# Optimization experiments

Hardware: AMD Instinct MI355X
Metric: run time of the kernel (lower is better)

Reference implementation:

```python
import jax, jax.numpy as jnp
import numpy as np

NUM_QUERIES = 10000
NUM_CLASSES = 2048
IOU_THRESH = 0.5


def setup_inputs() -> dict:
    key = jax.random.key(0)
    k1, k2, k3, k4 = jax.random.split(key, 4)
    return {
        "pred_logits": jax.random.normal(k1, (1, NUM_QUERIES, NUM_CLASSES), dtype=jnp.float32),
        "pred_boxes": jax.random.uniform(k2, (1, NUM_QUERIES, 4), dtype=jnp.float32),
        "cls_logits": jax.random.normal(k3, (1, NUM_CLASSES), dtype=jnp.float32),
        "target_sizes": jax.random.randint(k4, (1, 2), 480, 1333, dtype=jnp.int64),
    }


def box_cxcywh_to_xyxy(b):
    cx, cy, w, h = b[..., 0], b[..., 1], b[..., 2], b[..., 3]
    return jnp.stack([cx - 0.5 * w, cy - 0.5 * h, cx + 0.5 * w, cy + 0.5 * h], axis=-1)


def nms_keep(boxes, scores, iou_thresh):
    """Greedy NMS; returns a boolean keep mask over the N boxes (xyxy)."""
    n = boxes.shape[0]
    order = jnp.argsort(-scores)
    bs = boxes[order]  # [N,4] sorted by score desc
    areas = jnp.clip(bs[:, 2] - bs[:, 0], 0.0) * jnp.clip(bs[:, 3] - bs[:, 1], 0.0)
    idx = jnp.arange(n)

    def body(i, state):
        keep_s, active = state
        alive = active[i]
        keep_s = keep_s.at[i].set(alive)
        # IoU of box i against all boxes
        lt = jnp.maximum(bs[i, :2], bs[:, :2])
        rb = jnp.minimum(bs[i, 2:], bs[:, 2:])
        wh = jnp.clip(rb - lt, 0.0)
        inter = wh[:, 0] * wh[:, 1]
        iou = inter / (areas[i] + areas - inter)
        suppress = (iou > iou_thresh) & (idx > i) & alive
        return keep_s, active & (~suppress)

    keep_s, _ = jax.lax.fori_loop(
        0, n, body, (jnp.zeros(n, dtype=bool), jnp.ones(n, dtype=bool))
    )
    # map back from sorted order to original order
    return jnp.zeros(n, dtype=bool).at[order].set(keep_s)


def reference(pred_logits, pred_boxes, cls_logits, target_sizes):
    # class scores / labels
    prob = jax.nn.softmax(pred_logits, axis=-1)          # [B,Q,C]
    scores = prob.max(axis=-1)                           # [B,Q]
    labels = prob.argmax(axis=-1)                        # [B,Q]
    cls_preds = jnp.argmax(cls_logits, axis=1)           # [B]

    # boxes: cxcywh -> xyxy, clamp to [0,1], scale to image size
    boxes = jnp.clip(box_cxcywh_to_xyxy(pred_boxes), 0.0, 1.0)  # [B,Q,4]
    ts = target_sizes.astype(jnp.float32)
    img_h, img_w = ts[:, 0], ts[:, 1]
    scale_fct = jnp.stack([img_w, img_h, img_w, img_h], axis=1)  # [B,4]
    boxes = boxes * scale_fct[:, None, :]

    # greedy NMS on batch 0 (module only supports this path for B=1)
    keep = nms_keep(boxes[0], scores.reshape(-1), IOU_THRESH)    # [Q] bool

    return scores[0], labels[0], boxes[0], keep, cls_preds
```

## Files before the change

### kernel.cpp

```cpp
#include <hip/hip_runtime.h>
#include <stdint.h>

#define NQ 10000
#define NC 2048
#define NW 157
#define IOU_TH 0.5f


__global__ __launch_bounds__(256) void k_scores(const float* __restrict__ logits,
        float* __restrict__ out_scores, float* __restrict__ out_labels,
        float* __restrict__ ws_scores) {
    int wave = threadIdx.x >> 6;
    int lane = threadIdx.x & 63;
    int q = blockIdx.x * 4 + wave;
    if (q >= NQ) return;
    const float* row = logits + (size_t)q * NC;
    float4 v[8];
    float m = -3.4e38f;
    int am = 0;
    #pragma unroll
    for (int k = 0; k < 8; k++) {
        int idx = k * 256 + lane * 4;
        v[k] = *(const float4*)(row + idx);
        if (v[k].x > m) { m = v[k].x; am = idx; }
        if (v[k].y > m) { m = v[k].y; am = idx + 1; }
        if (v[k].z > m) { m = v[k].z; am = idx + 2; }
        if (v[k].w > m) { m = v[k].w; am = idx + 3; }
    }
    #pragma unroll
    for (int off = 32; off >= 1; off >>= 1) {
        float om = __shfl_xor(m, off);
        int   oa = __shfl_xor(am, off);
        if (om > m || (om == m && oa < am)) { m = om; am = oa; }
    }
    float s = 0.f;
    #pragma unroll
    for (int k = 0; k < 8; k++) {
        s += expf(v[k].x - m);
        s += expf(v[k].y - m);
        s += expf(v[k].z - m);
        s += expf(v[k].w - m);
    }
    #pragma unroll
    for (int off = 32; off >= 1; off >>= 1) s += __shfl_xor(s, off);
    if (lane == 0) {
        float sc = 1.0f / s;
        out_scores[q] = sc;
        out_labels[q] = (float)am;
        ws_scores[q]  = sc;
    }
}

__global__ __launch_bounds__(256) void k_cls(const float* __restrict__ cls,
                                             float* __restrict__ out) {
    float m = -3.4e38f; int am = 0x7fffffff;
    for (int idx = threadIdx.x; idx < NC; idx += 256) {
        float x = cls[idx];
        if (x > m) { m = x; am = idx; }
    }
    int lane = threadIdx.x & 63, wave = threadIdx.x >> 6;
    #pragma unroll
    for (int off = 32; off >= 1; off >>= 1) {
        float om = __shfl_xor(m, off); int oa = __shfl_xor(am, off);
        if (om > m || (om == m && oa < am)) { m = om; am = oa; }
    }
    __shared__ float sm[4]; __shared__ int sa[4];
    if (lane == 0) { sm[wave] = m; sa[wave] = am; }
    __syncthreads();
    if (threadIdx.x == 0) {
        for (int w = 1; w < 4; w++)
            if (sm[w] > m || (sm[w] == m && sa[w] < am)) { m = sm[w]; am = sa[w]; }
        out[0] = (float)am;
    }
}

__global__ __launch_bounds__(256) void k_boxes(const float* __restrict__ pb,
        const int* __restrict__ ts, float* __restrict__ out_boxes,
        float* __restrict__ boxes4, int* __restrict__ rank) {
    #pragma clang fp contract(off)
    int i = blockIdx.x * 256 + threadIdx.x;
    if (i >= NQ) return;
    rank[i] = 0;
    int a0 = ts[0], a1 = ts[1];
    int ih, iw;
    if (a1 == 0) { ih = a0; iw = ts[2]; } else { ih = a0; iw = a1; }
    float sh = (float)ih, sw = (float)iw;
    float4 b = *(const float4*)(pb + i * 4);
    float x1 = b.x - 0.5f * b.z;
    float y1 = b.y - 0.5f * b.w;
    float x2 = b.x + 0.5f * b.z;
    float y2 = b.y + 0.5f * b.w;
    x1 = fminf(fmaxf(x1, 0.f), 1.f) * sw;
    y1 = fminf(fmaxf(y1, 0.f), 1.f) * sh;
    x2 = fminf(fmaxf(x2, 0.f), 1.f) * sw;
    y2 = fminf(fmaxf(y2, 0.f), 1.f) * sh;
    float4 o = make_float4(x1, y1, x2, y2);
    *(float4*)(out_boxes + i * 4) = o;
    *(float4*)(boxes4 + i * 4) = o;
}

__global__ __launch_bounds__(256) void k_count(const float* __restrict__ scores,
                                               int* __restrict__ rank) {
    __shared__ float sc[2000];
    int jbase = blockIdx.y * 2000;
    int jn = min(2000, NQ - jbase);
    for (int t = threadIdx.x; t < jn; t += 256) sc[t] = scores[jbase + t];
    __syncthreads();
    int i = blockIdx.x * 256 + threadIdx.x;
    if (i >= NQ) return;
    float si = scores[i];
    int cnt = 0;
    for (int jj = 0; jj < jn; jj++) {
        float sj = sc[jj];
        int j = jbase + jj;
        cnt += (sj > si) || (sj == si && j < i);
    }
    if (cnt) atomicAdd(&rank[i], cnt);
}

__global__ __launch_bounds__(256) void k_scatter(const float* __restrict__ boxes4,
        const int* __restrict__ rank, int* __restrict__ order,
        float* __restrict__ sx1, float* __restrict__ sy1,
        float* __restrict__ sx2, float* __restrict__ sy2,
        float* __restrict__ sarea) {
    #pragma clang fp contract(off)
    int i = blockIdx.x * 256 + threadIdx.x;
    if (i >= NQ) return;
    int r = rank[i];
    order[r] = i;
    float4 b = *(const float4*)(boxes4 + i * 4);
    sx1[r] = b.x; sy1[r] = b.y; sx2[r] = b.z; sy2[r] = b.w;
    sarea[r] = fmaxf(b.z - b.x, 0.f) * fmaxf(b.w - b.y, 0.f);
}

__global__ __launch_bounds__(64) void k_mask(const float* __restrict__ sx1,
        const float* __restrict__ sy1, const float* __restrict__ sx2,
        const float* __restrict__ sy2, const float* __restrict__ sarea,
        unsigned long long* __restrict__ mask) {
    #pragma clang fp contract(off)
    int rb = blockIdx.x, cb = blockIdx.y;
    if (cb < rb) return;
    int t = threadIdx.x;
    __shared__ float cx1[64], cy1[64], cx2[64], cy2[64], ca[64];
    int j0 = cb * 64 + t;
    if (j0 < NQ) { cx1[t]=sx1[j0]; cy1[t]=sy1[j0]; cx2[t]=sx2[j0]; cy2[t]=sy2[j0]; ca[t]=sarea[j0]; }
    __syncthreads();
    int i = rb * 64 + t;
    if (i >= NQ) return;
    float xi1 = sx1[i], yi1 = sy1[i], xi2 = sx2[i], yi2 = sy2[i], ai = sarea[i];
    int ncol = min(64, NQ - cb * 64);
    unsigned long long word = 0;
    for (int jj = 0; jj < ncol; jj++) {
        int j = cb * 64 + jj;
        float lx = fmaxf(xi1, cx1[jj]);
        float ly = fmaxf(yi1, cy1[jj]);
        float rx = fminf(xi2, cx2[jj]);
        float ry = fminf(yi2, cy2[jj]);
        float w = fmaxf(rx - lx, 0.f);
        float h = fmaxf(ry - ly, 0.f);
        float inter = w * h;
        float denom = (ai + ca[jj]) - inter;
        float iou = inter / denom;
        bool sup = (iou > IOU_TH) && (j > i);
        word |= ((unsigned long long)(sup ? 1u : 0u)) << jj;
    }
    mask[(size_t)i * NW + cb] = word;
}

__global__ __launch_bounds__(256, 1) void k_scan(const unsigned long long* __restrict__ mask,
        const int* __restrict__ order, float* __restrict__ out_keep) {
    __shared__ unsigned long long rem[NW];
    __shared__ unsigned long long keepw[NW];
    __shared__ unsigned long long sh_kept;

    const int tid  = threadIdx.x;
    const int wave = tid >> 6;
    const int lane = tid & 63;

    for (int w = tid; w < NW; w += 256) rem[w] = 0;

    uint32_t dg_lo = 0, dg_hi = 0;
    if (wave == 0) {
        uint64_t dg = mask[(size_t)lane * NW + 0];
        dg_lo = (uint32_t)dg; dg_hi = (uint32_t)(dg >> 32);
    }
    __syncthreads();

    for (int c = 0; c < NW; c++) {
        if (wave == 0) {
            uint64_t t64 = rem[c];
            uint32_t clo = (uint32_t)__builtin_amdgcn_readfirstlane((int)(uint32_t)t64);
            uint32_t chi = (uint32_t)__builtin_amdgcn_readfirstlane((int)(uint32_t)(t64 >> 32));
            uint64_t cur = ((uint64_t)chi << 32) | clo;

            int nvalid = min(64, NQ - c * 64);
            if (nvalid < 64) cur |= (~0ull) << nvalid;

            uint64_t alive = ~cur;
            uint64_t kept  = 0;
            while (alive) {
                int b = (int)__builtin_ctzll(alive);
                uint32_t dlo = (uint32_t)__builtin_amdgcn_readlane((int)dg_lo, b);
                uint32_t dhi = (uint32_t)__builtin_amdgcn_readlane((int)dg_hi, b);
                uint64_t d = ((uint64_t)dhi << 32) | dlo;
                kept  |= 1ull << b;
                cur   |= d;
                alive &= ~(d | (1ull << b));
            }
            if (tid == 0) { sh_kept = kept; keepw[c] = cur; }
        }
        __syncthreads();

        uint64_t kt;
        {
            uint64_t t64 = sh_kept;
            uint32_t klo = (uint32_t)__builtin_amdgcn_readfirstlane((int)(uint32_t)t64);
            uint32_t khi = (uint32_t)__builtin_amdgcn_readfirstlane((int)(uint32_t)(t64 >> 32));
            kt = ((uint64_t)khi << 32) | klo;
        }

        uint64_t dg_n = 0;
        if (wave == 0 && c + 1 < NW) {
            int i2 = (c + 1) * 64 + lane;
            if (i2 < NQ) dg_n = mask[(size_t)i2 * NW + (c + 1)];
        }

        int w = c + 1 + tid;
        if (w < NW && kt) {
            const unsigned long long* base = mask + (size_t)c * 64 * NW + w;
            uint64_t acc = 0;
            uint64_t km = kt;
            while (km) {
                uint64_t a0 = 0, a1 = 0, a2 = 0, a3 = 0, a4 = 0, a5 = 0, a6 = 0, a7 = 0;
                if (km) { int r = (int)__builtin_ctzll(km); km &= km - 1; a0 = base[(size_t)r * NW]; }
                if (km) { int r = (int)__builtin_ctzll(km); km &= km - 1; a1 = base[(size_t)r * NW]; }
                if (km) { int r = (int)__builtin_ctzll(km); km &= km - 1; a2 = base[(size_t)r * NW]; }
                if (km) { int r = (int)__builtin_ctzll(km); km &= km - 1; a3 = base[(size_t)r * NW]; }
                if (km) { int r = (int)__builtin_ctzll(km); km &= km - 1; a4 = base[(size_t)r * NW]; }
                if (km) { int r = (int)__builtin_ctzll(km); km &= km - 1; a5 = base[(size_t)r * NW]; }
                if (km) { int r = (int)__builtin_ctzll(km); km &= km - 1; a6 = base[(size_t)r * NW]; }
                if (km) { int r = (int)__builtin_ctzll(km); km &= km - 1; a7 = base[(size_t)r * NW]; }
                acc |= (a0 | a1) | (a2 | a3) | ((a4 | a5) | (a6 | a7));
            }
            if (acc) rem[w] |= acc;
        }
        __syncthreads();

        if (wave == 0) { dg_lo = (uint32_t)dg_n; dg_hi = (uint32_t)(dg_n >> 32); }
    }

    for (int si = tid; si < NQ; si += 256) {
        unsigned long long kw = keepw[si >> 6];
        out_keep[order[si]] = ((kw >> (si & 63)) & 1ull) ? 0.f : 1.f;
    }
}

extern "C" void kernel_launch(void* const* d_in, const int* in_sizes, int n_in,
                              void* d_out, int out_size, void* d_ws, size_t ws_size,
                              hipStream_t stream) {
    const float* pred_logits = (const float*)d_in[0];
    const float* pred_boxes  = (const float*)d_in[1];
    const float* cls_logits  = (const float*)d_in[2];
    const int*   tsizes      = (const int*)d_in[3];

    float* out = (float*)d_out;
    float* out_scores = out;
    float* out_labels = out + 10000;
    float* out_boxes  = out + 20000;
    float* out_keep   = out + 60000;
    float* out_cls    = out + 70000;

    char* ws = (char*)d_ws;
    float* ws_scores = (float*)(ws + 0);
    int*   rank      = (int*)  (ws + 40000);
    float* boxes4    = (float*)(ws + 80000);
    float* sx1       = (float*)(ws + 240000);
    float* sy1       = (float*)(ws + 280000);
    float* sx2       = (float*)(ws + 320000);
    float* sy2       = (float*)(ws + 360000);
    float* sarea     = (float*)(ws + 400000);
    int*   order     = (int*)  (ws + 440000);
    unsigned long long* mask = (unsigned long long*)(ws + 480000);

    k_scores<<<2500, 256, 0, stream>>>(pred_logits, out_scores, out_labels, ws_scores);
    k_cls<<<1, 256, 0, stream>>>(cls_logits, out_cls);
    k_boxes<<<40, 256, 0, stream>>>(pred_boxes, tsizes, out_boxes, boxes4, rank);
    k_count<<<dim3(40, 5), 256, 0, stream>>>(ws_scores, rank);
    k_scatter<<<40, 256, 0, stream>>>(boxes4, rank, order, sx1, sy1, sx2, sy2, sarea);
    k_mask<<<dim3(157, 157), 64, 0, stream>>>(sx1, sy1, sx2, sy2, sarea, mask);
    k_scan<<<1, 256, 0, stream>>>(mask, order, out_keep);
}
```

Measured before the change: 497.3 us.

## Pipeline NMS scan by deferring far-column mask loads and prefetching next block

```diff
diff --git a/kernel.cpp b/kernel.cpp
--- a/kernel.cpp
+++ b/kernel.cpp
@@ -171,6 +171,8 @@
         const int* __restrict__ order, float* __restrict__ out_keep) {
     __shared__ unsigned long long rem[NW];
     __shared__ unsigned long long keepw[NW];
+    __shared__ unsigned long long dgbuf[2][64];
+    __shared__ unsigned long long ccbuf[2][64];
     __shared__ unsigned long long sh_kept;
 
     const int tid  = threadIdx.x;
@@ -179,74 +181,119 @@
 
     for (int w = tid; w < NW; w += 256) rem[w] = 0;
 
-    uint32_t dg_lo = 0, dg_hi = 0;
     if (wave == 0) {
-        uint64_t dg = mask[(size_t)lane * NW + 0];
-        dg_lo = (uint32_t)dg; dg_hi = (uint32_t)(dg >> 32);
+        const unsigned long long* rp = mask + (size_t)lane * NW;
+        dgbuf[0][lane] = rp[0];
+        ccbuf[0][lane] = rp[1];
     }
     __syncthreads();
 
+    uint64_t p0=0,p1=0,p2=0,p3=0,p4=0,p5=0,p6=0,p7=0;
+    uint64_t p8=0,p9=0,p10=0,p11=0,p12=0,p13=0,p14=0,p15=0;
+    uint64_t pextra = 0;
+    int pw = -1;
+
     for (int c = 0; c < NW; c++) {
+        uint64_t dn = 0, ccn = 0;
         if (wave == 0) {
+            if (c + 1 < NW) {
+                int i2 = (c + 1) * 64 + lane;
+                if (i2 < NQ) {
+                    const unsigned long long* rp = mask + (size_t)i2 * NW;
+                    dn = rp[c + 1];
+                    if (c + 2 < NW) ccn = rp[c + 2];
+                }
+            }
             uint64_t t64 = rem[c];
             uint32_t clo = (uint32_t)__builtin_amdgcn_readfirstlane((int)(uint32_t)t64);
             uint32_t chi = (uint32_t)__builtin_amdgcn_readfirstlane((int)(uint32_t)(t64 >> 32));
             uint64_t cur = ((uint64_t)chi << 32) | clo;
-
             int nvalid = min(64, NQ - c * 64);
             if (nvalid < 64) cur |= (~0ull) << nvalid;
+
+            uint64_t dgv = dgbuf[c & 1][lane];
+            uint32_t dvlo = (uint32_t)dgv, dvhi = (uint32_t)(dgv >> 32);
 
             uint64_t alive = ~cur;
             uint64_t kept  = 0;
             while (alive) {
                 int b = (int)__builtin_ctzll(alive);
-                uint32_t dlo = (uint32_t)__builtin_amdgcn_readlane((int)dg_lo, b);
-                uint32_t dhi = (uint32_t)__builtin_amdgcn_readlane((int)dg_hi, b);
+                uint32_t dlo = (uint32_t)__builtin_amdgcn_readlane((int)dvlo, b);
+                uint32_t dhi = (uint32_t)__builtin_amdgcn_readlane((int)dvhi, b);
                 uint64_t d = ((uint64_t)dhi << 32) | dlo;
                 kept  |= 1ull << b;
                 cur   |= d;
                 alive &= ~(d | (1ull << b));
             }
             if (tid == 0) { sh_kept = kept; keepw[c] = cur; }
+        } else {
+            if (pw >= 0) {
+                uint64_t pacc = ((p0|p1)|(p2|p3)) | ((p4|p5)|(p6|p7));
+                pacc |= ((p8|p9)|(p10|p11)) | ((p12|p13)|(p14|p15));
+                pacc |= pextra;
+                if (pacc) atomicOr(&rem[pw], (unsigned long long)pacc);
+            }
+            pw = -1;
         }
         __syncthreads();
 
-        uint64_t kt;
+        uint64_t kts;
         {
             uint64_t t64 = sh_kept;
             uint32_t klo = (uint32_t)__builtin_amdgcn_readfirstlane((int)(uint32_t)t64);
             uint32_t khi = (uint32_t)__builtin_amdgcn_readfirstlane((int)(uint32_t)(t64 >> 32));
-            kt = ((uint64_t)khi << 32) | klo;
+            kts = ((uint64_t)khi << 32) | klo;
         }
 
-        uint64_t dg_n = 0;
-        if (wave == 0 && c + 1 < NW) {
-            int i2 = (c + 1) * 64 + lane;
-            if (i2 < NQ) dg_n = mask[(size_t)i2 * NW + (c + 1)];
-        }
-
-        int w = c + 1 + tid;
-        if (w < NW && kt) {
-            const unsigned long long* base = mask + (size_t)c * 64 * NW + w;
-            uint64_t acc = 0;
-            uint64_t km = kt;
-            while (km) {
-                uint64_t a0 = 0, a1 = 0, a2 = 0, a3 = 0, a4 = 0, a5 = 0, a6 = 0, a7 = 0;
-                if (km) { int r = (int)__builtin_ctzll(km); km &= km - 1; a0 = base[(size_t)r * NW]; }
-                if (km) { int r = (int)__builtin_ctzll(km); km &= km - 1; a1 = base[(size_t)r * NW]; }
-                if (km) { int r = (int)__builtin_ctzll(km); km &= km - 1; a2 = base[(size_t)r * NW]; }
-                if (km) { int r = (int)__builtin_ctzll(km); km &= km - 1; a3 = base[(size_t)r * NW]; }
-                if (km) { int r = (int)__builtin_ctzll(km); km &= km - 1; a4 = base[(size_t)r * NW]; }
-                if (km) { int r = (int)__builtin_ctzll(km); km &= km - 1; a5 = base[(size_t)r * NW]; }
-                if (km) { int r = (int)__builtin_ctzll(km); km &= km - 1; a6 = base[(size_t)r * NW]; }
-                if (km) { int r = (int)__builtin_ctzll(km); km &= km - 1; a7 = base[(size_t)r * NW]; }
-                acc |= (a0 | a1) | (a2 | a3) | ((a4 | a5) | (a6 | a7));
-            }
-            if (acc) rem[w] |= acc;
+        if (wave == 0) {
+            if (c + 1 < NW) {
+                uint64_t ccv = ccbuf[c & 1][lane];
+                if ((kts >> lane) & 1ull) atomicOr(&rem[c + 1], (unsigned long long)ccv);
+                dgbuf[(c + 1) & 1][lane] = dn;
+                if (c + 2 < NW) ccbuf[(c + 1) & 1][lane] = ccn;
+            }
+        } else {
+            int w = c + 2 + (tid - 64);
+            if (kts && w < NW) {
+                const unsigned long long* base = mask + (size_t)(c * 64) * NW + w;
+                uint64_t km = kts;
+                int r_first = (int)__builtin_ctzll(km);
+                int r;
+                r = km ? (int)__builtin_ctzll(km) : r_first; if (km) km &= km - 1; p0  = base[(size_t)r * NW];
+                r = km ? (int)__builtin_ctzll(km) : r_first; if (km) km &= km - 1; p1  = base[(size_t)r * NW];
+                r = km ? (int)__builtin_ctzll(km) : r_first; if (km) km &= km - 1; p2  = base[(size_t)r * NW];
+                r = km ? (int)__builtin_ctzll(km) : r_first; if (km) km &= km - 1; p3  = base[(size_t)r * NW];
+                r = km ? (int)__builtin_ctzll(km) : r_first; if (km) km &= km - 1; p4  = base[(size_t)r * NW];
+                r = km ? (int)__builtin_ctzll(km) : r_first; if (km) km &= km - 1; p5  = base[(size_t)r * NW];
+                r = km ? (int)__builtin_ctzll(km) : r_first; if (km) km &= km - 1; p6  = base[(size_t)r * NW];
+                r = km ? (int)__builtin_ctzll(km) : r_first; if (km) km &= km - 1; p7  = base[(size_t)r * NW];
+                r = km ? (int)__builtin_ctzll(km) : r_first; if (km) km &= km - 1; p8  = base[(size_t)r * NW];
+                r = km ? (int)__builtin_ctzll(km) : r_first; if (km) km &= km - 1; p9  = base[(size_t)r * NW];
+                r = km ? (int)__builtin_ctzll(km) : r_first; if (km) km &= km - 1; p10 = base[(size_t)r * NW];
+                r = km ? (int)__builtin_ctzll(km) : r_first; if (km) km &= km - 1; p11 = base[(size_t)r * NW];
+                r = km ? (int)__builtin_ctzll(km) : r_first; if (km) km &= km - 1; p12 = base[(size_t)r * NW];
+                r = km ? (int)__builtin_ctzll(km) : r_first; if (km) km &= km - 1; p13 = base[(size_t)r * NW];
+                r = km ? (int)__builtin_ctzll(km) : r_first; if (km) km &= km - 1; p14 = base[(size_t)r * NW];
+                r = km ? (int)__builtin_ctzll(km) : r_first; if (km) km &= km - 1; p15 = base[(size_t)r * NW];
+                pextra = 0;
+                while (km) {
+                    uint64_t x0=0,x1=0,x2=0,x3=0,x4=0,x5=0,x6=0,x7=0;
+                    if (km) { r=(int)__builtin_ctzll(km); km&=km-1; x0=base[(size_t)r*NW]; }
+                    if (km) { r=(int)__builtin_ctzll(km); km&=km-1; x1=base[(size_t)r*NW]; }
+                    if (km) { r=(int)__builtin_ctzll(km); km&=km-1; x2=base[(size_t)r*NW]; }
+                    if (km) { r=(int)__builtin_ctzll(km); km&=km-1; x3=base[(size_t)r*NW]; }
+                    if (km) { r=(int)__builtin_ctzll(km); km&=km-1; x4=base[(size_t)r*NW]; }
+                    if (km) { r=(int)__builtin_ctzll(km); km&=km-1; x5=base[(size_t)r*NW]; }
+                    if (km) { r=(int)__builtin_ctzll(km); km&=km-1; x6=base[(size_t)r*NW]; }
+                    if (km) { r=(int)__builtin_ctzll(km); km&=km-1; x7=base[(size_t)r*NW]; }
+                    pextra |= (x0|x1)|(x2|x3)|((x4|x5)|(x6|x7));
+                }
+                pw = w;
+            } else {
+                pw = -1; pextra = 0;
+            }
         }
         __syncthreads();
-
-        if (wave == 0) { dg_lo = (uint32_t)dg_n; dg_hi = (uint32_t)(dg_n >> 32); }
     }
 
     for (int si = tid; si < NQ; si += 256) {
```

Result: faster. 429.9 us (-13.5%).

## Process two NMS mask blocks per scan round with pipelined suppression loads

Applied to the files above, without the earlier changes.

```diff
diff --git a/kernel.cpp b/kernel.cpp
--- a/kernel.cpp
+++ b/kernel.cpp
@@ -4,6 +4,7 @@
 #define NQ 10000
 #define NC 2048
 #define NW 157
+#define NR 79
 #define IOU_TH 0.5f
 
 
@@ -167,11 +168,19 @@
     mask[(size_t)i * NW + cb] = word;
 }
 
+__device__ __forceinline__ unsigned long long bcast64(unsigned long long v) {
+    uint32_t lo = (uint32_t)__builtin_amdgcn_readfirstlane((int)(uint32_t)v);
+    uint32_t hi = (uint32_t)__builtin_amdgcn_readfirstlane((int)(uint32_t)(v >> 32));
+    return ((unsigned long long)hi << 32) | lo;
+}
+
 __global__ __launch_bounds__(256, 1) void k_scan(const unsigned long long* __restrict__ mask,
         const int* __restrict__ order, float* __restrict__ out_keep) {
     __shared__ unsigned long long rem[NW];
     __shared__ unsigned long long keepw[NW];
-    __shared__ unsigned long long sh_kept;
+    __shared__ unsigned long long stA[2][4][64];
+    __shared__ unsigned long long stB[2][3][64];
+    __shared__ unsigned long long sh_k0, sh_k1;
 
     const int tid  = threadIdx.x;
     const int wave = tid >> 6;
@@ -179,74 +188,187 @@
 
     for (int w = tid; w < NW; w += 256) rem[w] = 0;
 
-    uint32_t dg_lo = 0, dg_hi = 0;
-    if (wave == 0) {
-        uint64_t dg = mask[(size_t)lane * NW + 0];
-        dg_lo = (uint32_t)dg; dg_hi = (uint32_t)(dg >> 32);
+    if (wave == 1) {
+        uint64_t sA0=0,sA1=0,sA2=0,sA3=0,sB0=0,sB1=0,sB2=0;
+        int ra = lane, rb = 64 + lane;
+        {
+            const unsigned long long* rp = mask + (size_t)ra * NW;
+            sA0 = rp[0]; sA1 = rp[1]; sA2 = rp[2]; sA3 = rp[3];
+        }
+        {
+            const unsigned long long* rp = mask + (size_t)rb * NW;
+            sB0 = rp[1]; sB1 = rp[2]; sB2 = rp[3];
+        }
+        stA[0][0][lane]=sA0; stA[0][1][lane]=sA1; stA[0][2][lane]=sA2; stA[0][3][lane]=sA3;
+        stB[0][0][lane]=sB0; stB[0][1][lane]=sB1; stB[0][2][lane]=sB2;
     }
     __syncthreads();
 
-    for (int c = 0; c < NW; c++) {
+    uint64_t pp0=0,pp1=0,pp2=0,pp3=0,pp4=0,pp5=0,pp6=0,pp7=0;
+    uint64_t pp8=0,pp9=0,pp10=0,pp11=0,pp12=0,pp13=0,pp14=0,pp15=0;
+    uint64_t pp16=0,pp17=0,pp18=0,pp19=0,pp20=0,pp21=0,pp22=0,pp23=0;
+    uint64_t pp24=0,pp25=0,pp26=0,pp27=0,pp28=0,pp29=0,pp30=0,pp31=0;
+    uint64_t pex = 0;
+    int pw = -1;
+
+    uint64_t kept0 = 0, kept1 = 0;
+
+    for (int r = 0; r < NR; r++) {
+        const int a = 2 * r, b = a + 1;
+        const int par = r & 1;
+
+        uint64_t sA0=0,sA1=0,sA2=0,sA3=0,sB0=0,sB1=0,sB2=0;
+
         if (wave == 0) {
-            uint64_t t64 = rem[c];
-            uint32_t clo = (uint32_t)__builtin_amdgcn_readfirstlane((int)(uint32_t)t64);
-            uint32_t chi = (uint32_t)__builtin_amdgcn_readfirstlane((int)(uint32_t)(t64 >> 32));
-            uint64_t cur = ((uint64_t)chi << 32) | clo;
-
-            int nvalid = min(64, NQ - c * 64);
-            if (nvalid < 64) cur |= (~0ull) << nvalid;
-
-            uint64_t alive = ~cur;
-            uint64_t kept  = 0;
+            uint64_t remA_v = rem[a];
+            uint64_t remB_v = (b < NW) ? rem[b] : ~0ull;
+            uint64_t dgA = stA[par][0][lane];
+            uint64_t xAB = stA[par][1][lane];
+            uint64_t dgB = (b < NW) ? stB[par][0][lane] : 0;
+
+            uint64_t cur0 = bcast64(remA_v);
+            int nv0 = min(64, NQ - a * 64);
+            if (nv0 < 64) cur0 |= (~0ull) << nv0;
+            uint32_t dglo = (uint32_t)dgA, dghi = (uint32_t)(dgA >> 32);
+            uint32_t xlo  = (uint32_t)xAB, xhi  = (uint32_t)(xAB >> 32);
+            uint64_t alive = ~cur0;
+            uint64_t k0 = 0, AcB = 0;
             while (alive) {
-                int b = (int)__builtin_ctzll(alive);
-                uint32_t dlo = (uint32_t)__builtin_amdgcn_readlane((int)dg_lo, b);
-                uint32_t dhi = (uint32_t)__builtin_amdgcn_readlane((int)dg_hi, b);
-                uint64_t d = ((uint64_t)dhi << 32) | dlo;
-                kept  |= 1ull << b;
-                cur   |= d;
-                alive &= ~(d | (1ull << b));
-            }
-            if (tid == 0) { sh_kept = kept; keepw[c] = cur; }
+                int bb = (int)__builtin_ctzll(alive);
+                uint64_t d = ((uint64_t)(uint32_t)__builtin_amdgcn_readlane((int)dghi, bb) << 32)
+                           | (uint32_t)__builtin_amdgcn_readlane((int)dglo, bb);
+                uint64_t x = ((uint64_t)(uint32_t)__builtin_amdgcn_readlane((int)xhi, bb) << 32)
+                           | (uint32_t)__builtin_amdgcn_readlane((int)xlo, bb);
+                k0    |= 1ull << bb;
+                cur0  |= d;
+                AcB   |= x;
+                alive &= ~(d | (1ull << bb));
+            }
+            kept0 = k0;
+
+            uint64_t k1 = 0, cur1 = 0;
+            if (b < NW) {
+                cur1 = bcast64(remB_v) | AcB;
+                int nv1 = min(64, NQ - b * 64);
+                if (nv1 < 64) cur1 |= (~0ull) << nv1;
+                uint32_t blo = (uint32_t)dgB, bhi = (uint32_t)(dgB >> 32);
+                uint64_t alv = ~cur1;
+                while (alv) {
+                    int bb = (int)__builtin_ctzll(alv);
+                    uint64_t d = ((uint64_t)(uint32_t)__builtin_amdgcn_readlane((int)bhi, bb) << 32)
+                               | (uint32_t)__builtin_amdgcn_readlane((int)blo, bb);
+                    k1  |= 1ull << bb;
+                    cur1 |= d;
+                    alv &= ~(d | (1ull << bb));
+                }
+            }
+            kept1 = k1;
+            if (tid == 0) {
+                sh_k0 = k0; sh_k1 = k1;
+                keepw[a] = cur0;
+                if (b < NW) keepw[b] = cur1;
+            }
+        } else {
+            if (pw >= 0) {
+                uint64_t pacc = (((pp0|pp1)|(pp2|pp3)) | ((pp4|pp5)|(pp6|pp7)))
+                              | (((pp8|pp9)|(pp10|pp11)) | ((pp12|pp13)|(pp14|pp15)));
+                pacc |= (((pp16|pp17)|(pp18|pp19)) | ((pp20|pp21)|(pp22|pp23)))
+                      | (((pp24|pp25)|(pp26|pp27)) | ((pp28|pp29)|(pp30|pp31)));
+                pacc |= pex;
+                if (pacc) atomicOr(&rem[pw], (unsigned long long)pacc);
+            }
+            pw = -1;
+
+            if (wave == 1) {
+                int a2 = a + 2, b2 = a + 3;
+                int ra = a2 * 64 + lane, rb = b2 * 64 + lane;
+                if (a2 < NW && ra < NQ) {
+                    const unsigned long long* rp = mask + (size_t)ra * NW + a2;
+                    sA0 = rp[0];
+                    if (a2 + 1 < NW) sA1 = rp[1];
+                    if (a2 + 2 < NW) sA2 = rp[2];
+                    if (a2 + 3 < NW) sA3 = rp[3];
+                }
+                if (b2 < NW && rb < NQ) {
+                    const unsigned long long* rp = mask + (size_t)rb * NW + b2;
+                    sB0 = rp[0];
+                    if (b2 + 1 < NW) sB1 = rp[1];
+                    if (b2 + 2 < NW) sB2 = rp[2];
+                }
+            }
         }
         __syncthreads();
 
-        uint64_t kt;
-        {
-            uint64_t t64 = sh_kept;
-            uint32_t klo = (uint32_t)__builtin_amdgcn_readfirstlane((int)(uint32_t)t64);
-            uint32_t khi = (uint32_t)__builtin_amdgcn_readfirstlane((int)(uint32_t)(t64 >> 32));
-            kt = ((uint64_t)khi << 32) | klo;
-        }
-
-        uint64_t dg_n = 0;
-        if (wave == 0 && c + 1 < NW) {
-            int i2 = (c + 1) * 64 + lane;
-            if (i2 < NQ) dg_n = mask[(size_t)i2 * NW + (c + 1)];
-        }
-
-        int w = c + 1 + tid;
-        if (w < NW && kt) {
-            const unsigned long long* base = mask + (size_t)c * 64 * NW + w;
-            uint64_t acc = 0;
-            uint64_t km = kt;
-            while (km) {
-                uint64_t a0 = 0, a1 = 0, a2 = 0, a3 = 0, a4 = 0, a5 = 0, a6 = 0, a7 = 0;
-                if (km) { int r = (int)__builtin_ctzll(km); km &= km - 1; a0 = base[(size_t)r * NW]; }
-                if (km) { int r = (int)__builtin_ctzll(km); km &= km - 1; a1 = base[(size_t)r * NW]; }
-                if (km) { int r = (int)__builtin_ctzll(km); km &= km - 1; a2 = base[(size_t)r * NW]; }
-                if (km) { int r = (int)__builtin_ctzll(km); km &= km - 1; a3 = base[(size_t)r * NW]; }
-                if (km) { int r = (int)__builtin_ctzll(km); km &= km - 1; a4 = base[(size_t)r * NW]; }
-                if (km) { int r = (int)__builtin_ctzll(km); km &= km - 1; a5 = base[(size_t)r * NW]; }
-                if (km) { int r = (int)__builtin_ctzll(km); km &= km - 1; a6 = base[(size_t)r * NW]; }
-                if (km) { int r = (int)__builtin_ctzll(km); km &= km - 1; a7 = base[(size_t)r * NW]; }
-                acc |= (a0 | a1) | (a2 | a3) | ((a4 | a5) | (a6 | a7));
-            }
-            if (acc) rem[w] |= acc;
+        const int c2 = a + 2, c3 = a + 3;
+        if (wave == 0) {
+            if (c2 < NW) {
+                uint64_t vA2 = stA[par][2][lane];
+                uint64_t vB1 = (b < NW) ? stB[par][1][lane] : 0;
+                uint64_t m2 = (((kept0 >> lane) & 1ull) ? vA2 : 0)
+                            | (((kept1 >> lane) & 1ull) ? vB1 : 0);
+                uint64_t m3 = 0;
+                if (c3 < NW) {
+                    uint64_t vA3 = stA[par][3][lane];
+                    uint64_t vB2 = (b < NW) ? stB[par][2][lane] : 0;
+                    m3 = (((kept0 >> lane) & 1ull) ? vA3 : 0)
+                       | (((kept1 >> lane) & 1ull) ? vB2 : 0);
+                }
+                #pragma unroll
+                for (int off = 32; off >= 1; off >>= 1) {
+                    m2 |= __shfl_xor(m2, off);
+                    m3 |= __shfl_xor(m3, off);
+                }
+                if (lane == 0) {
+                    rem[c2] |= m2;
+                    if (c3 < NW) rem[c3] |= m3;
+                }
+            }
+        } else {
+            uint64_t k0 = bcast64(sh_k0);
+            uint64_t k1 = bcast64(sh_k1);
+
+            if (wave == 1) {
+                int par2 = (r + 1) & 1;
+                stA[par2][0][lane]=sA0; stA[par2][1][lane]=sA1;
+                stA[par2][2][lane]=sA2; stA[par2][3][lane]=sA3;
+                stB[par2][0][lane]=sB0; stB[par2][1][lane]=sB1; stB[par2][2][lane]=sB2;
+            }
+
+            int w = a + 4 + (tid - 64);
+            if ((k0 | k1) && w < NW) {
+                const unsigned long long* baseA = mask + (size_t)(a * 64) * NW + w;
+                const unsigned long long* baseB = mask + (size_t)(b * 64) * NW + w;
+                uint64_t km0 = k0, km1 = k1;
+                const unsigned long long* fb =
+                    km0 ? baseA + (size_t)__builtin_ctzll(km0) * NW
+                        : baseB + (size_t)__builtin_ctzll(km1) * NW;
+                #define BULK_SLOT(P) { const unsigned long long* rp; \
+                    if (km0)      { rp = baseA + (size_t)__builtin_ctzll(km0) * NW; km0 &= km0 - 1; } \
+                    else if (km1) { rp = baseB + (size_t)__builtin_ctzll(km1) * NW; km1 &= km1 - 1; } \
+                    else rp = fb; \
+                    P = rp[0]; }
+                BULK_SLOT(pp0)  BULK_SLOT(pp1)  BULK_SLOT(pp2)  BULK_SLOT(pp3)
+                BULK_SLOT(pp4)  BULK_SLOT(pp5)  BULK_SLOT(pp6)  BULK_SLOT(pp7)
+                BULK_SLOT(pp8)  BULK_SLOT(pp9)  BULK_SLOT(pp10) BULK_SLOT(pp11)
+                BULK_SLOT(pp12) BULK_SLOT(pp13) BULK_SLOT(pp14) BULK_SLOT(pp15)
+                BULK_SLOT(pp16) BULK_SLOT(pp17) BULK_SLOT(pp18) BULK_SLOT(pp19)
+                BULK_SLOT(pp20) BULK_SLOT(pp21) BULK_SLOT(pp22) BULK_SLOT(pp23)
+                BULK_SLOT(pp24) BULK_SLOT(pp25) BULK_SLOT(pp26) BULK_SLOT(pp27)
+                BULK_SLOT(pp28) BULK_SLOT(pp29) BULK_SLOT(pp30) BULK_SLOT(pp31)
+                pex = 0;
+                while (km0 | km1) {
+                    uint64_t x0,x1,x2,x3,x4,x5,x6,x7;
+                    BULK_SLOT(x0) BULK_SLOT(x1) BULK_SLOT(x2) BULK_SLOT(x3)
+                    BULK_SLOT(x4) BULK_SLOT(x5) BULK_SLOT(x6) BULK_SLOT(x7)
+                    pex |= (x0|x1)|(x2|x3)|((x4|x5)|(x6|x7));
+                }
+                #undef BULK_SLOT
+                pw = w;
+            } else {
+                pw = -1; pex = 0;
+            }
         }
         __syncthreads();
-
-        if (wave == 0) { dg_lo = (uint32_t)dg_n; dg_hi = (uint32_t)(dg_n >> 32); }
     }
 
     for (int si = tid; si < NQ; si += 256) {
```

New measurement: 440.6 us. 11.4% less time.
